# Performance work log

Hardware: AMD Instinct MI355X
Metric: run time of the kernel (lower is better)

## Reference

```python
import jax, jax.numpy as jnp
import numpy as np
from jax import lax
import math

B, CH, BINS, CROP = 8, 2, 1024, 1024
NUM_BANDS = 4
FF = 2048
EPS = 1e-5
SCALE = 0.02  # weight init scale for numeric stability


def _inorm(x, g, b):
    # InstanceNorm2d: x [B, C, H, W], normalize over (H, W) per (B, C); biased var
    m = x.mean(axis=(2, 3), keepdims=True)
    v = x.var(axis=(2, 3), keepdims=True)
    return (x - m) / jnp.sqrt(v + EPS) * g[None, :, None, None] + b[None, :, None, None]


def _dwconv(x, k):
    # depthwise conv1d: x [B, bins, W], k [bins, 1, 3], padding=1, groups=bins
    return lax.conv_general_dilated(x, k, (1,), [(1, 1)],
                                    dimension_numbers=('NCH', 'OIH', 'NCH'),
                                    feature_group_count=x.shape[1])


def setup_inputs() -> dict:
    key = jax.random.key(0)
    ks = jax.random.split(key, 12)
    inp = {
        'x': jax.random.normal(ks[0], (B, CH, BINS, CROP), jnp.float32),
        'prev_qk': jax.random.normal(ks[1], (B, NUM_BANDS, CROP, CROP), jnp.float32),
        'g_in': jnp.ones((CROP,), jnp.float32),
        'b_in': jnp.zeros((CROP,), jnp.float32),
        'W_in': jax.random.normal(ks[2], (1, CH), jnp.float32) * SCALE,
        'bias_in': jnp.zeros((1,), jnp.float32),
        'g1': jnp.ones((CROP,), jnp.float32),
        'b1': jnp.zeros((CROP,), jnp.float32),
        'Wq': jax.random.normal(ks[3], (BINS, BINS), jnp.float32) * SCALE,
        'Wk': jax.random.normal(ks[4], (BINS, BINS), jnp.float32) * SCALE,
        'Wv': jax.random.normal(ks[5], (BINS, BINS), jnp.float32) * SCALE,
        'Wo': jax.random.normal(ks[6], (BINS, BINS), jnp.float32) * SCALE,
        'kq': jax.random.normal(ks[7], (BINS, 1, 3), jnp.float32) * SCALE,
        'kk': jax.random.normal(ks[8], (BINS, 1, 3), jnp.float32) * SCALE,
        'kv': jax.random.normal(ks[9], (BINS, 1, 3), jnp.float32) * SCALE,
        'pos_w': jax.random.normal(ks[10], (BINS // NUM_BANDS, CROP), jnp.float32) * SCALE,
        'g2': jnp.ones((CROP,), jnp.float32),
        'b2': jnp.zeros((CROP,), jnp.float32),
        'W_ff': jax.random.normal(ks[11], (1, 2), jnp.float32) * SCALE,
        'bias_ff': jnp.zeros((1,), jnp.float32),
        'W1': jax.random.normal(jax.random.fold_in(key, 100), (FF, BINS), jnp.float32) * SCALE,
        'W2': jax.random.normal(jax.random.fold_in(key, 101), (BINS, FF), jnp.float32) * SCALE,
    }
    return inp


def reference(x, prev_qk, g_in, b_in, W_in, bias_in, g1, b1, Wq, Wk, Wv, Wo,
              kq, kk, kv, pos_w, g2, b2, W_ff, bias_ff, W1, W2):
    b = x.shape[0]
    nb = NUM_BANDS
    hd = BINS // nb
    # in_norm + in_project: transposed layout [B, CROP, BINS, CH]
    xt = jnp.transpose(x, (0, 3, 2, 1))
    xt = _inorm(xt, g_in, b_in)
    xt = jnp.einsum('bwhc,oc->bwho', xt, W_in) + bias_in  # [B,CROP,BINS,1]
    x0 = jnp.transpose(xt, (0, 3, 2, 1))                  # [B,1,BINS,CROP]
    # norm1 + attention over frames (w == CROP, c == BINS)
    h = jnp.transpose(_inorm(jnp.transpose(x0, (0, 3, 2, 1)), g1, b1), (0, 3, 2, 1))
    a_in = jnp.transpose(h, (0, 3, 2, 1))[..., 0]         # [B, W, BINS]
    q = jnp.einsum('bwc,oc->bwo', a_in, Wq)
    q = jnp.transpose(_dwconv(jnp.transpose(q, (0, 2, 1)), kq), (0, 2, 1))
    k = jnp.einsum('bwc,oc->bwo', a_in, Wk)
    k = jnp.transpose(_dwconv(jnp.transpose(k, (0, 2, 1)), kk), (0, 2, 1))
    v = jnp.einsum('bwc,oc->bwo', a_in, Wv)
    v = jnp.transpose(_dwconv(jnp.transpose(v, (0, 2, 1)), kv), (0, 2, 1))
    q4 = jnp.transpose(q.reshape(b, CROP, nb, hd), (0, 2, 1, 3))   # [B,nb,W,hd]
    k4 = jnp.transpose(k.reshape(b, CROP, nb, hd), (0, 2, 3, 1))   # [B,nb,hd,W]
    v4 = jnp.transpose(v.reshape(b, CROP, nb, hd), (0, 2, 1, 3))   # [B,nb,W,hd]
    # relative-position bias via pad-and-shift
    p = jnp.matmul(q4, pos_w)                                      # [B,nb,W,CROP]
    p = jnp.pad(p, ((0, 0), (0, 0), (0, 0), (1, 0)))
    p = jnp.swapaxes(p, 2, 3)[:, :, 1:, :]                         # [B,nb,CROP,W]
    qk = (jnp.matmul(q4, k4) + p) / math.sqrt(BINS)
    qk = qk + prev_qk
    a = jax.nn.softmax(qk, axis=-1)
    o = jnp.transpose(jnp.matmul(a, v4), (0, 2, 1, 3)).reshape(b, CROP, BINS)
    o = jnp.einsum('bwc,oc->bwo', o, Wo)                           # [B,W,BINS]
    h4 = jnp.transpose(o[..., None], (0, 3, 2, 1))                 # [B,1,BINS,CROP]
    x1 = jnp.concatenate([x0, h4], axis=1)                         # [B,2,BINS,CROP]
    # norm2 + ff_project + squared-ReLU FFN
    hn = _inorm(jnp.transpose(x1, (0, 3, 2, 1)), g2, b2)           # [B,CROP,BINS,2]
    hn = jnp.einsum('bwhc,oc->bwho', hn, W_ff) + bias_ff           # [B,CROP,BINS,1]
    hn = jnp.transpose(hn, (0, 3, 2, 1))                           # [B,1,BINS,CROP]
    ht = jnp.swapaxes(hn, 2, 3)                                    # [B,1,CROP,BINS]
    ht = jnp.square(jax.nn.relu(jnp.einsum('bowc,fc->bowf', ht, W1)))
    ht = jnp.einsum('bowf,cf->bowc', ht, W2)
    hf = jnp.swapaxes(ht, 2, 3)                                    # [B,1,BINS,CROP]
    out = jnp.concatenate([x1, hf], axis=1)                        # [B,3,BINS,CROP]
    return out, qk
```

## Files before the change

kernel.cpp:

```cpp
#include <hip/hip_runtime.h>
#include <stdint.h>

#define DEVI __device__ __forceinline__

typedef __attribute__((ext_vector_type(8))) short bf16x8;
typedef __attribute__((ext_vector_type(4))) float f32x4;

#define B_    8
#define CROP_ 1024
#define BINS_ 1024
#define NB_   4
#define HD_   256
#define FF_   2048
#define EPSF  1e-5f
#define OUT0_ELEMS (8ull*3ull*1024ull*1024ull)
#define MBYTE (1024ull*1024ull)
#define M1ELEM (1024ll*1024ll)
#define SMCAP 8.0f

DEVI unsigned short f2bf(float f) {
  unsigned u = __builtin_bit_cast(unsigned, f);
  u += 0x7fffu + ((u >> 16) & 1u);
  return (unsigned short)(u >> 16);
}
DEVI float bf2f(unsigned short h) {
  unsigned u = ((unsigned)h) << 16;
  return __builtin_bit_cast(float, u);
}

DEVI void gload16(const unsigned short* g, unsigned short* l) {
  __builtin_amdgcn_global_load_lds(
      (const __attribute__((address_space(1))) unsigned int*)g,
      (__attribute__((address_space(3))) unsigned int*)l, 16, 0, 0);
}

__global__ __launch_bounds__(256) void k_conv_all(
    const float* __restrict__ Wq, const float* __restrict__ Wk,
    const float* __restrict__ Wv, const float* __restrict__ Wo,
    const float* __restrict__ W1, const float* __restrict__ W2,
    const float* __restrict__ pw,
    unsigned short* __restrict__ WQKVB, unsigned short* __restrict__ WOB,
    unsigned short* __restrict__ W1B, unsigned short* __restrict__ W2B,
    unsigned short* __restrict__ PWT) {
  long long i4 = ((long long)blockIdx.x*256 + threadIdx.x)*4;
  long long stride4 = (long long)gridDim.x*256*4;
  for (; i4 < 8*M1ELEM; i4 += stride4) {
    float4 v;
    unsigned short* dst;
    if (i4 < 3*M1ELEM) {
      const float* s = i4 < M1ELEM ? Wq : (i4 < 2*M1ELEM ? Wk : Wv);
      v = *(const float4*)&s[i4 & (M1ELEM-1)];
      dst = &WQKVB[i4];
    } else if (i4 < 4*M1ELEM) { v = *(const float4*)&Wo[i4-3*M1ELEM]; dst = &WOB[i4-3*M1ELEM]; }
    else if (i4 < 6*M1ELEM)   { v = *(const float4*)&W1[i4-4*M1ELEM]; dst = &W1B[i4-4*M1ELEM]; }
    else                      { v = *(const float4*)&W2[i4-6*M1ELEM]; dst = &W2B[i4-6*M1ELEM]; }
    ushort4 o;
    o.x = f2bf(v.x); o.y = f2bf(v.y); o.z = f2bf(v.z); o.w = f2bf(v.w);
    *(ushort4*)dst = o;
  }
  for (long long j = (long long)blockIdx.x*256 + threadIdx.x; j < (1ll << 18);
       j += (long long)gridDim.x*256) {
    int w = (int)(j >> 8), d = (int)(j & 255);
    PWT[j] = f2bf(pw[d*1024 + w]);
  }
}

__global__ __launch_bounds__(256) void k_instx0(const float* __restrict__ x,
    const float* __restrict__ g_in, const float* __restrict__ b_in,
    const float* __restrict__ W_in, const float* __restrict__ bias_in,
    const float* __restrict__ g1, const float* __restrict__ b1,
    float* __restrict__ outp, float* __restrict__ x0t,
    unsigned short* __restrict__ ain) {
  int b = blockIdx.y, w0 = blockIdx.x*32;
  int t = threadIdx.x, wl = t & 31, p = t >> 5;
  const float* xb = x + (size_t)b*2*M1ELEM + w0 + wl;
  float s = 0.f, ss = 0.f;
  for (int i = p*256; i < p*256 + 256; ++i) {
    float v = xb[(size_t)i*CROP_];
    s += v; ss += v*v;
  }
  __shared__ float ls[8][32], lss[8][32];
  __shared__ float s_coef[32], s_add[32];
  __shared__ float s_cm[32], s_ca[32];
  ls[p][wl] = s; lss[p][wl] = ss;
  __syncthreads();
  float W0 = W_in[0], W1 = W_in[1], bi = bias_in[0];
  float sW = W0 + W1;
  if (t < 32) {
    float S = 0.f, SS = 0.f;
    for (int q = 0; q < 8; ++q) { S += ls[q][t]; SS += lss[q][t]; }
    float m = S*(1.f/2048.f);
    float var = SS*(1.f/2048.f) - m*m;
    float r = rsqrtf(var + EPSF);
    int w = w0 + t;
    float coef = r*g_in[w];
    s_coef[t] = coef;
    s_add[t] = b_in[w]*sW + bi - coef*m*sW;
  }
  __syncthreads();
  __shared__ float tile[32][33];
  int tx = wl, ty = p;
  float coef = s_coef[tx], add = s_add[tx];
  int w = w0 + tx;
  float s1 = 0.f, ss1 = 0.f;
  for (int h0 = 0; h0 < BINS_; h0 += 32) {
#pragma unroll
    for (int q = 0; q < 4; ++q) {
      int h = h0 + ty + q*8;
      size_t i0 = ((size_t)b*2*BINS_ + h)*CROP_ + w;
      float val = coef*(W0*x[i0] + W1*x[i0 + (size_t)M1ELEM]) + add;
      outp[(((size_t)b*3)*BINS_ + h)*CROP_ + w] = val;
      tile[ty + q*8][tx] = val;
      s1 += val; ss1 += val*val;
    }
    __syncthreads();
#pragma unroll
    for (int q = 0; q < 4; ++q)
      x0t[((size_t)b*CROP_ + w0 + ty + q*8)*BINS_ + h0 + tx] = tile[tx][ty + q*8];
    __syncthreads();
  }
  ls[p][wl] = s1; lss[p][wl] = ss1;
  __syncthreads();
  if (t < 32) {
    float S = 0.f, SS = 0.f;
    for (int q = 0; q < 8; ++q) { S += ls[q][t]; SS += lss[q][t]; }
    float m = S*(1.f/1024.f);
    float var = SS*(1.f/1024.f) - m*m;
    float rs = rsqrtf(var + EPSF);
    int ww = w0 + t;
    float cm = rs*g1[ww];
    s_cm[t] = cm;
    s_ca[t] = b1[ww] - m*cm;
  }
  __syncthreads();
  for (int wloc = 0; wloc < 32; ++wloc) {
    float cm = s_cm[wloc], ca = s_ca[wloc];
    const float* row = x0t + ((size_t)b*CROP_ + w0 + wloc)*BINS_;
    float4 v = *(const float4*)&row[t*4];
    ushort4 o;
    o.x = f2bf(v.x*cm + ca);
    o.y = f2bf(v.y*cm + ca);
    o.z = f2bf(v.z*cm + ca);
    o.w = f2bf(v.w*cm + ca);
    *(ushort4*)&ain[((size_t)b*CROP_ + w0 + wloc)*BINS_ + t*4] = o;
  }
}

__global__ __launch_bounds__(256) void k_norm2(const float* __restrict__ x0t,
    const float* __restrict__ o2,
    const float* __restrict__ g2, const float* __restrict__ b2,
    const float* __restrict__ W_ff, const float* __restrict__ bias_ff,
    unsigned short* __restrict__ hn) {
  int r = blockIdx.x;
  int w = r & (CROP_ - 1);
  int t = threadIdx.x;
  const float* ra = x0t + (size_t)r*BINS_;
  const float* rb = o2 + (size_t)r*BINS_;
  float4 va = *(const float4*)&ra[t*4];
  float4 vb = *(const float4*)&rb[t*4];
  float s = va.x + va.y + va.z + va.w + vb.x + vb.y + vb.z + vb.w;
  float ss = va.x*va.x + va.y*va.y + va.z*va.z + va.w*va.w
           + vb.x*vb.x + vb.y*vb.y + vb.z*vb.z + vb.w*vb.w;
  for (int off = 32; off; off >>= 1) { s += __shfl_xor(s, off); ss += __shfl_xor(ss, off); }
  __shared__ float red[8];
  int wv = t >> 6;
  if ((t & 63) == 0) { red[wv] = s; red[4 + wv] = ss; }
  __syncthreads();
  s = red[0] + red[1] + red[2] + red[3];
  ss = red[4] + red[5] + red[6] + red[7];
  float m = s*(1.f/2048.f);
  float var = ss*(1.f/2048.f) - m*m;
  float rs = rsqrtf(var + EPSF);
  float W0 = W_ff[0], W1f = W_ff[1];
  float gg = g2[w]*rs;
  float add = b2[w]*(W0 + W1f) + bias_ff[0] - gg*m*(W0 + W1f);
  ushort4 o;
  o.x = f2bf(gg*(W0*va.x + W1f*vb.x) + add);
  o.y = f2bf(gg*(W0*va.y + W1f*vb.y) + add);
  o.z = f2bf(gg*(W0*va.z + W1f*vb.z) + add);
  o.w = f2bf(gg*(W0*va.w + W1f*vb.w) + add);
  *(ushort4*)&hn[(size_t)r*BINS_ + t*4] = o;
}

__global__ __launch_bounds__(256) void k_dwconv(const unsigned short* __restrict__ qkvb,
    const float* __restrict__ kq, const float* __restrict__ kk2,
    unsigned short* __restrict__ qkvc) {
  int w = blockIdx.x, b = blockIdx.y, which = blockIdx.z;
  int t = threadIdx.x;
  const float* kw = which == 0 ? kq : kk2;
  const unsigned short* r0 = qkvb + (size_t)which*8*M1ELEM + ((size_t)b*CROP_ + w)*BINS_;
  unsigned short* d0 = qkvc + (size_t)which*8*M1ELEM + ((size_t)b*CROP_ + w)*BINS_;
  int c4 = t*4;
  float kf[12];
  *(float4*)&kf[0] = *(const float4*)&kw[c4*3];
  *(float4*)&kf[4] = *(const float4*)&kw[c4*3 + 4];
  *(float4*)&kf[8] = *(const float4*)&kw[c4*3 + 8];
  ushort4 vm = *(const ushort4*)&r0[c4];
  ushort4 va = make_ushort4(0,0,0,0), vbn = make_ushort4(0,0,0,0);
  if (w > 0)        va  = *(const ushort4*)&r0[c4 - BINS_];
  if (w < CROP_-1)  vbn = *(const ushort4*)&r0[c4 + BINS_];
  const unsigned short* vmp = (const unsigned short*)&vm;
  const unsigned short* vap = (const unsigned short*)&va;
  const unsigned short* vbp = (const unsigned short*)&vbn;
  ushort4 o;
  unsigned short* op = (unsigned short*)&o;
#pragma unroll
  for (int j = 0; j < 4; ++j) {
    float acc = bf2f(vmp[j])*kf[3*j + 1] + bf2f(vap[j])*kf[3*j] + bf2f(vbp[j])*kf[3*j + 2];
    op[j] = f2bf(acc);
  }
  *(ushort4*)&d0[c4] = o;
}

__global__ __launch_bounds__(256) void k_dwconv_trV(const unsigned short* __restrict__ vb,
    const float* __restrict__ kv, unsigned short* __restrict__ vct) {
  int b = blockIdx.z;
  int w0 = blockIdx.x*32, c0 = blockIdx.y*32;
  int tx = threadIdx.x, ty = threadIdx.y;
  __shared__ unsigned short tile[34][33];
  const unsigned short* S = vb + (size_t)b*M1ELEM;
#pragma unroll
  for (int q = 0; q < 4; ++q) {
    int wl = ty + q*8;
    tile[wl + 1][tx] = S[(size_t)(w0 + wl)*BINS_ + c0 + tx];
  }
  if (ty == 0) tile[0][tx]  = (w0 > 0)          ? S[(size_t)(w0 - 1)*BINS_ + c0 + tx] : (unsigned short)0;
  if (ty == 1) tile[33][tx] = (w0 + 32 < CROP_) ? S[(size_t)(w0 + 32)*BINS_ + c0 + tx] : (unsigned short)0;
  __syncthreads();
  unsigned short* D = vct + (size_t)b*M1ELEM;
#pragma unroll
  for (int q = 0; q < 4; ++q) {
    int cl = ty + q*8;
    int c = c0 + cl;
    float k0 = kv[c*3], k1 = kv[c*3 + 1], k2 = kv[c*3 + 2];
    float val = k0*bf2f(tile[tx][cl]) + k1*bf2f(tile[tx + 1][cl]) + k2*bf2f(tile[tx + 2][cl]);
    D[(size_t)c*CROP_ + w0 + tx] = f2bf(val);
  }
}

#define BUFB 49152

template<int AC, int BC, int ABY>
DEVI void stage_gen(const unsigned short* Ab, int lda, const unsigned short* Bb, int ldb,
                    int k0, unsigned short* buf, int t, int wv) {
  int trow = t >> 3;
  int colel = ((t & 7) ^ (trow & 7)) << 3;
  unsigned short* lbase = buf + wv*512;
  const unsigned short* ga = Ab + (size_t)trow*lda + k0 + colel;
#pragma unroll
  for (int c = 0; c < AC; ++c)
    gload16(ga + (size_t)(c*64)*lda, lbase + c*4096);
  const unsigned short* gb = Bb + (size_t)trow*ldb + k0 + colel;
  unsigned short* lbb = buf + ABY/2 + wv*512;
#pragma unroll
  for (int c = 0; c < BC; ++c)
    gload16(gb + (size_t)(c*64)*ldb, lbb + c*4096);
}

#define RING_BODY(BOFF, ...)                                                           \
    bf16x8 af[2][4], bf[2][4];                                                         \
    _Pragma("unroll")                                                                  \
    for (int kk = 0; kk < 2; ++kk) {                                                   \
      _Pragma("unroll")                                                                \
      for (int mi = 0; mi < 4; ++mi) {                                                 \
        int row = wm*64 + mi*16 + lr;                                                  \
        af[kk][mi] = *(const bf16x8*)(bufc + ((row*128 + kk*64 + lk*16) ^ sx));        \
      }                                                                                \
      _Pragma("unroll")                                                                \
      for (int ni = 0; ni < 4; ++ni) {                                                 \
        int row = wn*64 + ni*16 + lr;                                                  \
        bf[kk][ni] = *(const bf16x8*)(bufc + BOFF + ((row*128 + kk*64 + lk*16) ^ sx)); \
      }                                                                                \
    }                                                                                  \
    asm volatile("s_waitcnt lgkmcnt(0)" ::: "memory");                                 \
    __builtin_amdgcn_s_barrier();                                                      \
    __VA_ARGS__;                                                                       \
    __builtin_amdgcn_s_setprio(1);                                                     \
    _Pragma("unroll")                                                                  \
    for (int kk = 0; kk < 2; ++kk)                                                     \
      _Pragma("unroll")                                                                \
      for (int mi = 0; mi < 4; ++mi)                                                   \
        _Pragma("unroll")                                                              \
        for (int ni = 0; ni < 4; ++ni)                                                 \
          acc[mi][ni] = __builtin_amdgcn_mfma_f32_16x16x32_bf16(af[kk][mi], bf[kk][ni], acc[mi][ni], 0, 0, 0); \
    __builtin_amdgcn_s_setprio(0);                                                     \
    if (kt + 1 < NT) {                                                                 \
      int rem = (NT-1 < kt+3 ? NT-1 : kt+3) - (kt+1);                                  \
      if (rem >= 2)      asm volatile("s_waitcnt vmcnt(12)" ::: "memory");             \
      else if (rem == 1) asm volatile("s_waitcnt vmcnt(6)"  ::: "memory");             \
      else               asm volatile("s_waitcnt vmcnt(0)"  ::: "memory");             \
      __builtin_amdgcn_s_barrier();                                                    \
    }

template<int MODE>
__global__ __launch_bounds__(512) void k_gemm3(
    const unsigned short* __restrict__ A, int lda,
    const unsigned short* __restrict__ Bt, int ldb,
    void* __restrict__ C, int ldc, int K, float* __restrict__ C2, int ch)
{
  __shared__ __align__(16) unsigned short lds[3*24576];
  const unsigned short* Ab = A + (size_t)blockIdx.x*256*lda;
  const unsigned short* Bb = Bt + (size_t)blockIdx.y*128*ldb;
  const int t = threadIdx.x;
  const int wv = t >> 6, ln = t & 63;
  const int wm = wv >> 1, wn = wv & 1;
  const int lr = ln & 15, lk = ln >> 4;
  const int sx = (lr & 7) << 4;
  const int NT = K >> 6;
  stage_gen<4,2,32768>(Ab, lda, Bb, ldb, 0,   lds,           t, wv);
  stage_gen<4,2,32768>(Ab, lda, Bb, ldb, 64,  lds + 24576,   t, wv);
  stage_gen<4,2,32768>(Ab, lda, Bb, ldb, 128, lds + 49152,   t, wv);
  asm volatile("s_waitcnt vmcnt(12)" ::: "memory");
  __builtin_amdgcn_s_barrier();

  f32x4 acc[4][4] = {};
  for (int kt = 0; kt < NT; ++kt) {
    const int cur = kt % 3;
    const char* bufc = (const char*)lds + cur*BUFB;
    RING_BODY(32768,
      if (kt + 3 < NT) stage_gen<4,2,32768>(Ab, lda, Bb, ldb, (kt+3)*64,
                                            (unsigned short*)((char*)lds + cur*BUFB), t, wv))
  }

  if (MODE != 3) {
    const int row0 = blockIdx.x*256 + wm*64 + lk*4;
    const int col0 = blockIdx.y*128 + wn*64 + lr;
#pragma unroll
    for (int mi = 0; mi < 4; ++mi)
#pragma unroll
      for (int ni = 0; ni < 4; ++ni)
#pragma unroll
        for (int j = 0; j < 4; ++j) {
          int row = row0 + mi*16 + j;
          int col = col0 + ni*16;
          float v = acc[mi][ni][j];
          if (MODE == 0 || MODE == 4) {
            ((float*)C)[(size_t)row*ldc + col] = v;
          } else if (MODE == 2) {
            float rr = fmaxf(v, 0.f);
            ((unsigned short*)C)[(size_t)row*ldc + col] = f2bf(rr*rr);
          } else if (MODE == 5) {
            ((unsigned short*)C)[(size_t)(col >> 10)*8*M1ELEM + (size_t)row*1024 + (col & 1023)] = f2bf(v);
          }
        }
  }
  if (MODE == 3 || MODE == 4) {
    __syncthreads();
    float* ldsT = (float*)lds + wv*4160;
#pragma unroll
    for (int mi = 0; mi < 4; ++mi)
#pragma unroll
      for (int ni = 0; ni < 4; ++ni)
#pragma unroll
        for (int j = 0; j < 4; ++j)
          ldsT[(ni*16 + lr)*65 + mi*16 + lk*4 + j] = acc[mi][ni][j];
    asm volatile("s_waitcnt lgkmcnt(0)" ::: "memory");
    int l16 = ln & 15, csub = ln >> 4;
    int b = blockIdx.x >> 2;
    int wbase = ((blockIdx.x & 3) << 8) + wm*64 + l16*4;
    float* outc = C2 + (((size_t)b*3 + ch)*BINS_)*CROP_;
#pragma unroll
    for (int cb = 0; cb < 16; ++cb) {
      int cl = cb*4 + csub;
      float4 v4;
      v4.x = ldsT[cl*65 + l16*4 + 0];
      v4.y = ldsT[cl*65 + l16*4 + 1];
      v4.z = ldsT[cl*65 + l16*4 + 2];
      v4.w = ldsT[cl*65 + l16*4 + 3];
      *(float4*)&outc[(size_t)(blockIdx.y*128 + wn*64 + cl)*CROP_ + wbase] = v4;
    }
  }
}

DEVI void stage_qk(const unsigned short* qc_b, const unsigned short* kc_b,
                   const unsigned short* pwt, int bx, int by, int k0,
                   unsigned short* buf, int t, int wv) {
  int trow = t >> 3;
  int colel = ((t & 7) ^ (trow & 7)) << 3;
  unsigned short* lbase = buf + wv*512;
  if (k0 < 256) {
    const unsigned short* ga = qc_b + (size_t)(bx*256 + trow)*BINS_ + k0 + colel;
#pragma unroll
    for (int c = 0; c < 4; ++c)
      gload16(ga + (size_t)(c*64)*BINS_, lbase + c*4096);
  } else {
    const unsigned short* ga = pwt + (size_t)(bx*256 + trow)*HD_ + (k0 - 256) + colel;
#pragma unroll
    for (int c = 0; c < 4; ++c)
      gload16(ga + (size_t)(c*64)*HD_, lbase + c*4096);
  }
  const unsigned short* gbsrc = (k0 < 256) ? kc_b : qc_b;
  int kb = (k0 < 256) ? k0 : k0 - 256;
  const unsigned short* gb = gbsrc + (size_t)(by*128 + trow)*BINS_ + kb + colel;
  unsigned short* lbb = buf + 16384 + wv*512;
#pragma unroll
  for (int c = 0; c < 2; ++c)
    gload16(gb + (size_t)(c*64)*BINS_, lbb + c*4096);
}

__global__ __launch_bounds__(512) void k_qkpos2(
    const unsigned short* __restrict__ qc, const unsigned short* __restrict__ kc,
    const unsigned short* __restrict__ pwt,
    const float* __restrict__ prev, float* __restrict__ qkout,
    unsigned short* __restrict__ Pbuf, float* __restrict__ Lg)
{
  __shared__ __align__(16) unsigned short lds[3*24576];
  const int z = blockIdx.z, b = z >> 2, n = z & 3;
  const size_t bandoff = (size_t)b*CROP_*BINS_ + (size_t)n*HD_;
  const unsigned short* qc_b = qc + bandoff;
  const unsigned short* kc_b = kc + bandoff;
  const int bx = blockIdx.x, by = blockIdx.y;
  const int t = threadIdx.x;
  const int wv = t >> 6, ln = t & 63;
  const int wm = wv >> 1, wn = wv & 1;
  const int lr = ln & 15, lk = ln >> 4;
  const int sx = (lr & 7) << 4;
  const int NT = 8;
  stage_qk(qc_b, kc_b, pwt, bx, by, 0,   lds,         t, wv);
  stage_qk(qc_b, kc_b, pwt, bx, by, 64,  lds + 24576, t, wv);
  stage_qk(qc_b, kc_b, pwt, bx, by, 128, lds + 49152, t, wv);
  asm volatile("s_waitcnt vmcnt(12)" ::: "memory");
  __builtin_amdgcn_s_barrier();

  f32x4 acc[4][4] = {};
  for (int kt = 0; kt < NT; ++kt) {
    const int cur = kt % 3;
    const char* bufc = (const char*)lds + cur*BUFB;
    RING_BODY(32768,
      if (kt + 3 < NT) stage_qk(qc_b, kc_b, pwt, bx, by, (kt+3)*64,
                                (unsigned short*)((char*)lds + cur*BUFB), t, wv))
  }

  const float* pz = prev + (size_t)z*M1ELEM;
  float* oz = qkout + (size_t)z*M1ELEM;
  unsigned short* Pz = Pbuf + (size_t)z*M1ELEM;
  const int row0g = bx*256;
  const int col0 = by*128 + wn*64 + lr;
  float* slf = (float*)lds;
  const int rbase = wm*64 + lk*4;
#pragma unroll
  for (int mi = 0; mi < 4; ++mi) {
    float psum[4] = {0.f, 0.f, 0.f, 0.f};
#pragma unroll
    for (int ni = 0; ni < 4; ++ni)
#pragma unroll
      for (int j = 0; j < 4; ++j) {
        size_t idx = (size_t)(row0g + rbase + mi*16 + j)*CROP_ + col0 + ni*16;
        float val = acc[mi][ni][j]*0.03125f + pz[idx];
        oz[idx] = val;
        float p = __expf(val - SMCAP);
        Pz[idx] = f2bf(p);
        psum[j] += p;
      }
#pragma unroll
    for (int off = 1; off < 16; off <<= 1)
#pragma unroll
      for (int j = 0; j < 4; ++j) psum[j] += __shfl_xor(psum[j], off);
    if (lr == 0)
#pragma unroll
      for (int j = 0; j < 4; ++j) slf[wn*256 + rbase + mi*16 + j] = psum[j];
  }
  __syncthreads();
  if (t < 256) {
    size_t si = ((size_t)z*CROP_ + row0g + t)*8 + by;
    Lg[si] = slf[t] + slf[256 + t];
  }
}

__global__ __launch_bounds__(512) void k_pv3(
    const unsigned short* __restrict__ P, const float* __restrict__ Lg,
    const unsigned short* __restrict__ vct, unsigned short* __restrict__ ob)
{
  __shared__ __align__(16) unsigned short lds[3*24576];
  __shared__ float s_il[128];
  const int z = blockIdx.y, b = z >> 2, band = z & 3;
  const int bx = blockIdx.x;
  const unsigned short* Ab = P + (size_t)z*M1ELEM + (size_t)bx*128*CROP_;
  const unsigned short* Bb = vct + ((size_t)b*CROP_ + band*HD_)*CROP_;
  const int t = threadIdx.x;
  const int wv = t >> 6, ln = t & 63;
  const int wm = wv >> 2, wn = wv & 3;
  const int lr = ln & 15, lk = ln >> 4;
  const int sx = (lr & 7) << 4;
  const int NT = 16;
  if (t < 128) {
    size_t rg = (size_t)z*CROP_ + bx*128 + t;
    float l = 0.f;
#pragma unroll
    for (int cb = 0; cb < 8; ++cb) l += Lg[rg*8 + cb];
    s_il[t] = 1.f / l;
  }
  stage_gen<2,4,16384>(Ab, CROP_, Bb, CROP_, 0,   lds,         t, wv);
  stage_gen<2,4,16384>(Ab, CROP_, Bb, CROP_, 64,  lds + 24576, t, wv);
  stage_gen<2,4,16384>(Ab, CROP_, Bb, CROP_, 128, lds + 49152, t, wv);
  asm volatile("s_waitcnt vmcnt(12) lgkmcnt(0)" ::: "memory");
  __builtin_amdgcn_s_barrier();

  f32x4 acc[4][4] = {};
  for (int kt = 0; kt < NT; ++kt) {
    const int cur = kt % 3;
    const char* bufc = (const char*)lds + cur*BUFB;
    RING_BODY(16384,
      if (kt + 3 < NT) stage_gen<2,4,16384>(Ab, CROP_, Bb, CROP_, (kt+3)*64,
                                            (unsigned short*)((char*)lds + cur*BUFB), t, wv))
  }
#pragma unroll
  for (int mi = 0; mi < 4; ++mi)
#pragma unroll
    for (int j = 0; j < 4; ++j) {
      int rl = wm*64 + mi*16 + lk*4 + j;
      float il = s_il[rl];
#pragma unroll
      for (int ni = 0; ni < 4; ++ni) {
        int col = band*HD_ + wn*64 + ni*16 + lr;
        ob[((size_t)b*CROP_ + bx*128 + rl)*BINS_ + col] = f2bf(acc[mi][ni][j]*il);
      }
    }
}

extern "C" void kernel_launch(void* const* d_in, const int* in_sizes, int n_in,
                              void* d_out, int out_size, void* d_ws, size_t ws_size,
                              hipStream_t stream) {
  (void)in_sizes; (void)n_in; (void)out_size; (void)ws_size;
  const float* x       = (const float*)d_in[0];
  const float* prev_qk = (const float*)d_in[1];
  const float* g_in    = (const float*)d_in[2];
  const float* b_in    = (const float*)d_in[3];
  const float* W_in    = (const float*)d_in[4];
  const float* bias_in = (const float*)d_in[5];
  const float* g1      = (const float*)d_in[6];
  const float* b1      = (const float*)d_in[7];
  const float* Wq      = (const float*)d_in[8];
  const float* Wk      = (const float*)d_in[9];
  const float* Wv      = (const float*)d_in[10];
  const float* Wo      = (const float*)d_in[11];
  const float* kq      = (const float*)d_in[12];
  const float* kk      = (const float*)d_in[13];
  const float* kv      = (const float*)d_in[14];
  const float* pos_w   = (const float*)d_in[15];
  const float* g2      = (const float*)d_in[16];
  const float* b2      = (const float*)d_in[17];
  const float* W_ff    = (const float*)d_in[18];
  const float* bias_ff = (const float*)d_in[19];
  const float* W1      = (const float*)d_in[20];
  const float* W2      = (const float*)d_in[21];

  char* ws = (char*)d_ws;
  unsigned short* WQKVB = (unsigned short*)(ws + 0*MBYTE);
  unsigned short* WOB   = (unsigned short*)(ws + 6*MBYTE);
  unsigned short* W1B   = (unsigned short*)(ws + 8*MBYTE);
  unsigned short* W2B   = (unsigned short*)(ws + 12*MBYTE);
  unsigned short* PWT   = (unsigned short*)(ws + 16*MBYTE);
  float*          Lg    = (float*)(ws + 17*MBYTE);
  float*          X0T   = (float*)(ws + 20*MBYTE);
  unsigned short* AIN   = (unsigned short*)(ws + 52*MBYTE);
  unsigned short* QKVB  = (unsigned short*)(ws + 68*MBYTE);
  unsigned short* PBUF  = (unsigned short*)(ws + 52*MBYTE);
  unsigned short* QKVC  = (unsigned short*)(ws + 116*MBYTE);
  float*          O2    = (float*)(ws + 116*MBYTE);
  unsigned short* OB    = (unsigned short*)(ws + 148*MBYTE);
  unsigned short* VCT   = (unsigned short*)(ws + 164*MBYTE);
  unsigned short* HN    = (unsigned short*)(ws + 52*MBYTE);
  unsigned short* HT    = (unsigned short*)(ws + 20*MBYTE);

  float* outp  = (float*)d_out;
  float* qkout = outp + OUT0_ELEMS;

  dim3 blk256(256, 1, 1);
  dim3 blk512(512, 1, 1);
  dim3 blk32x8(32, 8, 1);

  k_conv_all<<<8448, blk256, 0, stream>>>(Wq, Wk, Wv, Wo, W1, W2, pos_w,
                                          WQKVB, WOB, W1B, W2B, PWT);
  k_instx0<<<dim3(32, 8, 1), blk256, 0, stream>>>(x, g_in, b_in, W_in, bias_in,
                                                  g1, b1, outp, X0T, AIN);
  k_gemm3<5><<<dim3(32, 24, 1), blk512, 0, stream>>>(AIN, 1024, WQKVB, 1024, QKVB, 0, 1024, nullptr, 0);
  k_dwconv<<<dim3(1024, 8, 2), blk256, 0, stream>>>(QKVB, kq, kk, QKVC);
  k_dwconv_trV<<<dim3(32, 32, 8), blk32x8, 0, stream>>>(QKVB + (size_t)2*8*M1ELEM, kv, VCT);
  k_qkpos2<<<dim3(4, 8, 32), blk512, 0, stream>>>(QKVC, QKVC + (size_t)8*M1ELEM, PWT,
                                                  prev_qk, qkout, PBUF, Lg);
  k_pv3<<<dim3(8, 32, 1), blk512, 0, stream>>>(PBUF, Lg, VCT, OB);
  k_gemm3<4><<<dim3(32, 8, 1), blk512, 0, stream>>>(OB, 1024, WOB, 1024, O2, 1024, 1024, outp, 1);
  k_norm2<<<8192, blk256, 0, stream>>>(X0T, O2, g2, b2, W_ff, bias_ff, HN);
  k_gemm3<2><<<dim3(32, 16, 1), blk512, 0, stream>>>(HN, 1024, W1B, 1024, HT, 2048, 1024, nullptr, 0);
  k_gemm3<3><<<dim3(32, 8, 1), blk512, 0, stream>>>(HT, 2048, W2B, 2048, nullptr, 1024, 2048, outp, 2);
}
```

Measured before the change: 447.6 us.

## Replace 256x128 GEMM kernel with 128x128 tile, 256-thread, K=32 pipelined GEMM

The 512-thread GEMM with a 256x128 output tile and 64-wide K steps is replaced by a 256-thread kernel with a 128x128 tile and 32-wide K steps. It uses a simpler unswizzled LDS staging routine and a three-stage ring, and the transpose epilogue now runs in two halves to fit the smaller LDS. The aim is more, smaller blocks for better CU occupancy and load balance, with less LDS per block. The trade-offs are less data reuse per tile, more barriers per unit of K, and possible LDS bank conflicts from the unswizzled layout.

Result: no change. 454.1 us (+1.5%).

```diff
diff --git a/kernel.cpp b/kernel.cpp
--- a/kernel.cpp
+++ b/kernel.cpp
@@ -292,39 +292,70 @@
       __builtin_amdgcn_s_barrier();                                                    \
     }
 
+DEVI void stage128(const unsigned short* Ab, int lda, const unsigned short* Bb, int ldb,
+                   int k0, unsigned short* buf, int t, int wv) {
+  int ln = t & 63;
+  int r = wv*16 + (ln >> 2);
+  int c8 = (ln & 3)*8;
+  gload16(Ab + (size_t)r*lda + k0 + c8,        buf + wv*512);
+  gload16(Ab + (size_t)(64 + r)*lda + k0 + c8, buf + 2048 + wv*512);
+  gload16(Bb + (size_t)r*ldb + k0 + c8,        buf + 4096 + wv*512);
+  gload16(Bb + (size_t)(64 + r)*ldb + k0 + c8, buf + 6144 + wv*512);
+}
+
 template<int MODE>
-__global__ __launch_bounds__(512) void k_gemm3(
+__global__ __launch_bounds__(256) void k_g128(
     const unsigned short* __restrict__ A, int lda,
     const unsigned short* __restrict__ Bt, int ldb,
     void* __restrict__ C, int ldc, int K, float* __restrict__ C2, int ch)
 {
-  __shared__ __align__(16) unsigned short lds[3*24576];
-  const unsigned short* Ab = A + (size_t)blockIdx.x*256*lda;
+  __shared__ __align__(16) unsigned short lds[3*8192];
+  const unsigned short* Ab = A + (size_t)blockIdx.x*128*lda;
   const unsigned short* Bb = Bt + (size_t)blockIdx.y*128*ldb;
   const int t = threadIdx.x;
   const int wv = t >> 6, ln = t & 63;
-  const int wm = wv >> 1, wn = wv & 1;
+  const int wr = (wv >> 1)*64, wc = (wv & 1)*64;
   const int lr = ln & 15, lk = ln >> 4;
-  const int sx = (lr & 7) << 4;
-  const int NT = K >> 6;
-  stage_gen<4,2,32768>(Ab, lda, Bb, ldb, 0,   lds,           t, wv);
-  stage_gen<4,2,32768>(Ab, lda, Bb, ldb, 64,  lds + 24576,   t, wv);
-  stage_gen<4,2,32768>(Ab, lda, Bb, ldb, 128, lds + 49152,   t, wv);
-  asm volatile("s_waitcnt vmcnt(12)" ::: "memory");
+  const int NT = K >> 5;
+  stage128(Ab, lda, Bb, ldb, 0,  lds,         t, wv);
+  stage128(Ab, lda, Bb, ldb, 32, lds + 8192,  t, wv);
+  stage128(Ab, lda, Bb, ldb, 64, lds + 16384, t, wv);
+  asm volatile("s_waitcnt vmcnt(8)" ::: "memory");
   __builtin_amdgcn_s_barrier();
 
   f32x4 acc[4][4] = {};
   for (int kt = 0; kt < NT; ++kt) {
     const int cur = kt % 3;
-    const char* bufc = (const char*)lds + cur*BUFB;
-    RING_BODY(32768,
-      if (kt + 3 < NT) stage_gen<4,2,32768>(Ab, lda, Bb, ldb, (kt+3)*64,
-                                            (unsigned short*)((char*)lds + cur*BUFB), t, wv))
+    const unsigned short* lA = lds + cur*8192;
+    const unsigned short* lB = lA + 4096;
+    bf16x8 af[4], bfr[4];
+#pragma unroll
+    for (int mi = 0; mi < 4; ++mi) af[mi]  = *(const bf16x8*)&lA[(wr + mi*16 + lr)*32 + lk*8];
+#pragma unroll
+    for (int ni = 0; ni < 4; ++ni) bfr[ni] = *(const bf16x8*)&lB[(wc + ni*16 + lr)*32 + lk*8];
+    asm volatile("s_waitcnt lgkmcnt(0)" ::: "memory");
+    __builtin_amdgcn_s_barrier();
+    if (kt + 3 < NT)
+      stage128(Ab, lda, Bb, ldb, (kt + 3)*32, lds + cur*8192, t, wv);
+    __builtin_amdgcn_s_setprio(1);
+#pragma unroll
+    for (int mi = 0; mi < 4; ++mi)
+#pragma unroll
+      for (int ni = 0; ni < 4; ++ni)
+        acc[mi][ni] = __builtin_amdgcn_mfma_f32_16x16x32_bf16(af[mi], bfr[ni], acc[mi][ni], 0, 0, 0);
+    __builtin_amdgcn_s_setprio(0);
+    if (kt + 1 < NT) {
+      int rem = (NT-1 < kt+3 ? NT-1 : kt+3) - (kt+1);
+      if (rem >= 2)      asm volatile("s_waitcnt vmcnt(8)" ::: "memory");
+      else if (rem == 1) asm volatile("s_waitcnt vmcnt(4)" ::: "memory");
+      else               asm volatile("s_waitcnt vmcnt(0)" ::: "memory");
+      __builtin_amdgcn_s_barrier();
+    }
   }
 
   if (MODE != 3) {
-    const int row0 = blockIdx.x*256 + wm*64 + lk*4;
-    const int col0 = blockIdx.y*128 + wn*64 + lr;
+    const int row0 = blockIdx.x*128 + wr + lk*4;
+    const int col0 = blockIdx.y*128 + wc + lr;
 #pragma unroll
     for (int mi = 0; mi < 4; ++mi)
 #pragma unroll
@@ -346,28 +377,35 @@
   }
   if (MODE == 3 || MODE == 4) {
     __syncthreads();
-    float* ldsT = (float*)lds + wv*4160;
-#pragma unroll
-    for (int mi = 0; mi < 4; ++mi)
-#pragma unroll
-      for (int ni = 0; ni < 4; ++ni)
-#pragma unroll
-        for (int j = 0; j < 4; ++j)
-          ldsT[(ni*16 + lr)*65 + mi*16 + lk*4 + j] = acc[mi][ni][j];
-    asm volatile("s_waitcnt lgkmcnt(0)" ::: "memory");
-    int l16 = ln & 15, csub = ln >> 4;
-    int b = blockIdx.x >> 2;
-    int wbase = ((blockIdx.x & 3) << 8) + wm*64 + l16*4;
+    float* ldsT = (float*)lds + wv*2112;
+    const int b = blockIdx.x >> 3;
+    const int wbase = ((blockIdx.x & 7) << 7) + wr + (ln & 15)*4;
+    const int csub = ln >> 4;
     float* outc = C2 + (((size_t)b*3 + ch)*BINS_)*CROP_;
 #pragma unroll
-    for (int cb = 0; cb < 16; ++cb) {
-      int cl = cb*4 + csub;
-      float4 v4;
-      v4.x = ldsT[cl*65 + l16*4 + 0];
-      v4.y = ldsT[cl*65 + l16*4 + 1];
-      v4.z = ldsT[cl*65 + l16*4 + 2];
-      v4.w = ldsT[cl*65 + l16*4 + 3];
-      *(float4*)&outc[(size_t)(blockIdx.y*128 + wn*64 + cl)*CROP_ + wbase] = v4;
+    for (int h = 0; h < 2; ++h) {
+#pragma unroll
+      for (int ni = 2*h; ni < 2*h + 2; ++ni) {
+        int colL = (ni - 2*h)*16 + lr;
+#pragma unroll
+        for (int mi = 0; mi < 4; ++mi)
+#pragma unroll
+          for (int j = 0; j < 4; ++j)
+            ldsT[colL*65 + mi*16 + lk*4 + j] = acc[mi][ni][j];
+      }
+      asm volatile("s_waitcnt lgkmcnt(0)" ::: "memory");
+#pragma unroll
+      for (int cb = 0; cb < 8; ++cb) {
+        int cl = cb*4 + csub;
+        float4 v4;
+        v4.x = ldsT[cl*65 + (ln & 15)*4 + 0];
+        v4.y = ldsT[cl*65 + (ln & 15)*4 + 1];
+        v4.z = ldsT[cl*65 + (ln & 15)*4 + 2];
+        v4.w = ldsT[cl*65 + (ln & 15)*4 + 3];
+        int colg = blockIdx.y*128 + wc + h*32 + cl;
+        *(float4*)&outc[(size_t)colg*CROP_ + wbase] = v4;
+      }
+      asm volatile("s_waitcnt lgkmcnt(0) vmcnt(0)" ::: "memory");
     }
   }
 }
@@ -574,14 +612,14 @@
                                           WQKVB, WOB, W1B, W2B, PWT);
   k_instx0<<<dim3(32, 8, 1), blk256, 0, stream>>>(x, g_in, b_in, W_in, bias_in,
                                                   g1, b1, outp, X0T, AIN);
-  k_gemm3<5><<<dim3(32, 24, 1), blk512, 0, stream>>>(AIN, 1024, WQKVB, 1024, QKVB, 0, 1024, nullptr, 0);
+  k_g128<5><<<dim3(64, 24, 1), blk256, 0, stream>>>(AIN, 1024, WQKVB, 1024, QKVB, 0, 1024, nullptr, 0);
   k_dwconv<<<dim3(1024, 8, 2), blk256, 0, stream>>>(QKVB, kq, kk, QKVC);
   k_dwconv_trV<<<dim3(32, 32, 8), blk32x8, 0, stream>>>(QKVB + (size_t)2*8*M1ELEM, kv, VCT);
   k_qkpos2<<<dim3(4, 8, 32), blk512, 0, stream>>>(QKVC, QKVC + (size_t)8*M1ELEM, PWT,
                                                   prev_qk, qkout, PBUF, Lg);
   k_pv3<<<dim3(8, 32, 1), blk512, 0, stream>>>(PBUF, Lg, VCT, OB);
-  k_gemm3<4><<<dim3(32, 8, 1), blk512, 0, stream>>>(OB, 1024, WOB, 1024, O2, 1024, 1024, outp, 1);
+  k_g128<4><<<dim3(64, 8, 1), blk256, 0, stream>>>(OB, 1024, WOB, 1024, O2, 1024, 1024, outp, 1);
   k_norm2<<<8192, blk256, 0, stream>>>(X0T, O2, g2, b2, W_ff, bias_ff, HN);
-  k_gemm3<2><<<dim3(32, 16, 1), blk512, 0, stream>>>(HN, 1024, W1B, 1024, HT, 2048, 1024, nullptr, 0);
-  k_gemm3<3><<<dim3(32, 8, 1), blk512, 0, stream>>>(HT, 2048, W2B, 2048, nullptr, 1024, 2048, outp, 2);
-}
+  k_g128<2><<<dim3(64, 16, 1), blk256, 0, stream>>>(HN, 1024, W1B, 1024, HT, 2048, 1024, nullptr, 0);
+  k_g128<3><<<dim3(64, 8, 1), blk256, 0, stream>>>(HT, 2048, W2B, 2048, nullptr, 1024, 2048, outp, 2);
+}
```
